# Optimization experiments

Hardware: AMD Instinct MI355X
Metric: run time of the kernel (lower is better)

## Reference

```python
import jax, jax.numpy as jnp
import numpy as np

N_NODES = 20000
N_EDGES = 320000
N_RELS = 500
EMB = 256
D4 = EMB // 4
B = 32
GAMMA = 12.0
BN_EPS = 1e-5


def _linear(x, W, b):
    return x @ W.T + b


def _bn(x, g, b, m, v):
    # BatchNorm1d in eval mode with running stats
    return (x - m) * jax.lax.rsqrt(v + BN_EPS) * g + b


def _comp_layer(src, dst, h, e, WO, bO, WI, bI, WS, bS, bng, bnb, bnm, bnv):
    # CompGCNLayer: u_sub_e message + per-node mean over in-edges ('ho')
    # and, on the reversed graph, over out-edges ('hi'); nodes with no
    # incident edges get 0 (dgl mean semantics).
    n = h.shape[0]
    ones = jnp.ones(src.shape[0], h.dtype)
    deg_in = jnp.maximum(jax.ops.segment_sum(ones, dst, num_segments=n), 1.0)
    deg_out = jnp.maximum(jax.ops.segment_sum(ones, src, num_segments=n), 1.0)
    ho = jax.ops.segment_sum(h[src] - e, dst, num_segments=n) / deg_in[:, None]
    hi = jax.ops.segment_sum(h[dst] - e, src, num_segments=n) / deg_out[:, None]
    out = (_linear(ho, WO, bO) + _linear(hi, WI, bI) + _linear(h, WS, bS)) / 3.0
    return _bn(out, bng, bnb, bnm, bnv)


def _forward(node_embs, edge_embs, params, src, dst, e_vid, hids, rids, tids,
             is_update_g_embs, is_head_pred):
    (W_O1, b_O1, W_I1, b_I1, W_S1, b_S1, bn1_g, bn1_b, bn1_m, bn1_v, Wr1, br1,
     W_O2, b_O2, W_I2, b_I2, W_S2, b_S2, bn2_g, bn2_b, bn2_m, bn2_v, Wr2, br2) = params
    if is_update_g_embs:
        he = edge_embs[e_vid]                                   # [E, D]
        h1 = jnp.tanh(_comp_layer(src, dst, node_embs, he,
                                  W_O1, b_O1, W_I1, b_I1, W_S1, b_S1,
                                  bn1_g, bn1_b, bn1_m, bn1_v))  # [N, D/4]
        he1 = jnp.tanh(_linear(he, Wr1, br1))                   # [E, D/4]
        hn = jnp.tanh(_comp_layer(src, dst, h1, he1,
                                  W_O2, b_O2, W_I2, b_I2, W_S2, b_S2,
                                  bn2_g, bn2_b, bn2_m, bn2_v))  # [N, D]
    else:
        hn = node_embs
    heads = hn[hids]
    tails = hn[tids]
    rels = _linear(jax.nn.relu(_linear(edge_embs[rids], Wr1, br1)), Wr2, br2)
    b = hids.shape[0]
    n = hn.shape[0]
    # Faithful to torch repeat_interleave indexing in predict():
    # flat element k pairs query row k//C with candidate row k//B.
    cand_idx = (jnp.arange(b)[:, None] * n + jnp.arange(n)[None, :]) // b  # [B, N]
    cand = hn[cand_idx]                                                    # [B, N, D]
    if is_head_pred == 1:
        diff = cand + (rels - tails)[:, None, :]
    else:
        diff = (heads + rels)[:, None, :] - cand
    dist = jnp.sqrt(jnp.sum(diff * diff, axis=-1))  # p = norm = 2
    score = jax.nn.sigmoid(GAMMA - dist)
    return hn, score


def setup_inputs() -> dict:
    key = jax.random.key(0)
    ks = jax.random.split(key, 20)
    w = lambda k, shp: jax.random.normal(k, shp, jnp.float32) * 0.05
    inp = {
        "node_embs": jax.random.normal(ks[0], (N_NODES, EMB), jnp.float32),
        "edge_embs": jax.random.normal(ks[1], (N_RELS, EMB), jnp.float32),
        "W_O1": w(ks[2], (D4, EMB)), "b_O1": jnp.zeros((D4,), jnp.float32),
        "W_I1": w(ks[3], (D4, EMB)), "b_I1": jnp.zeros((D4,), jnp.float32),
        "W_S1": w(ks[4], (D4, EMB)), "b_S1": jnp.zeros((D4,), jnp.float32),
        "bn1_g": jnp.ones((D4,), jnp.float32), "bn1_b": jnp.zeros((D4,), jnp.float32),
        "bn1_m": jnp.zeros((D4,), jnp.float32), "bn1_v": jnp.ones((D4,), jnp.float32),
        "Wr1": w(ks[5], (D4, EMB)), "br1": jnp.zeros((D4,), jnp.float32),
        "W_O2": w(ks[6], (EMB, D4)), "b_O2": jnp.zeros((EMB,), jnp.float32),
        "W_I2": w(ks[7], (EMB, D4)), "b_I2": jnp.zeros((EMB,), jnp.float32),
        "W_S2": w(ks[8], (EMB, D4)), "b_S2": jnp.zeros((EMB,), jnp.float32),
        "bn2_g": jnp.ones((EMB,), jnp.float32), "bn2_b": jnp.zeros((EMB,), jnp.float32),
        "bn2_m": jnp.zeros((EMB,), jnp.float32), "bn2_v": jnp.ones((EMB,), jnp.float32),
        "Wr2": w(ks[9], (EMB, D4)), "br2": jnp.zeros((EMB,), jnp.float32),
        "src": jax.random.randint(ks[10], (N_EDGES,), 0, N_NODES, jnp.int32),
        "dst": jax.random.randint(ks[11], (N_EDGES,), 0, N_NODES, jnp.int32),
        "e_vid": jax.random.randint(ks[12], (N_EDGES,), 0, N_RELS, jnp.int32),
        "hids": jax.random.randint(ks[13], (B,), 0, N_NODES, jnp.int32),
        "rids": jax.random.randint(ks[14], (B,), 0, N_RELS, jnp.int32),
        "tids": jax.random.randint(ks[15], (B,), 0, N_NODES, jnp.int32),
        "is_update_g_embs": 1,
        "is_head_pred": 0,
    }
    return inp


def reference(node_embs, edge_embs,
              W_O1, b_O1, W_I1, b_I1, W_S1, b_S1, bn1_g, bn1_b, bn1_m, bn1_v,
              Wr1, br1,
              W_O2, b_O2, W_I2, b_I2, W_S2, b_S2, bn2_g, bn2_b, bn2_m, bn2_v,
              Wr2, br2,
              src, dst, e_vid, hids, rids, tids,
              is_update_g_embs, is_head_pred):
    params = (W_O1, b_O1, W_I1, b_I1, W_S1, b_S1, bn1_g, bn1_b, bn1_m, bn1_v,
              Wr1, br1,
              W_O2, b_O2, W_I2, b_I2, W_S2, b_S2, bn2_g, bn2_b, bn2_m, bn2_v,
              Wr2, br2)
    return _forward(node_embs, edge_embs, params, src, dst, e_vid,
                    hids, rids, tids, is_update_g_embs, is_head_pred)
```

## Files before the change

kernel.cpp:

```cpp
#include <hip/hip_runtime.h>
#include <math.h>

#define NN 20000
#define NE 320000
#define NR 500
#define EMBD 256
#define D4 64
#define BQ 32
#define TOT (2 * NN)
#define NB 40

#define NBLK_HIST 1250
#define NBLK_BN 448
#define NBLK_K1 (NBLK_HIST + NBLK_BN + 2 + BQ)

#define NBLK_GC1 939
#define NBLK_GE1 32
#define NBLK_MEGA (NBLK_GC1 + NBLK_GE1 + NBLK_HIST)

typedef __attribute__((ext_vector_type(8))) short bf16x8;
typedef __attribute__((ext_vector_type(4))) float f32x4;

__device__ __forceinline__ unsigned short f2bf(float x)
{
    unsigned int u = __float_as_uint(x);
    unsigned int r = (u + 0x7fffu + ((u >> 16) & 1u)) >> 16;
    return (unsigned short)r;
}

__device__ __forceinline__ float4 bf4tof4(uint2 u)
{
    float4 r;
    r.x = __uint_as_float((u.x & 0xFFFFu) << 16);
    r.y = __uint_as_float(u.x & 0xFFFF0000u);
    r.z = __uint_as_float((u.y & 0xFFFFu) << 16);
    r.w = __uint_as_float(u.y & 0xFFFF0000u);
    return r;
}

__global__ __launch_bounds__(256) void k_prep(
    const int* __restrict__ src, const int* __restrict__ dst,
    const int* __restrict__ evid, int* __restrict__ cnt, unsigned* __restrict__ rank2,
    const float* __restrict__ W_O1, const float* __restrict__ W_I1,
    const float* __restrict__ W_S1, const float* __restrict__ Wr1,
    const float* __restrict__ W_O2, const float* __restrict__ W_I2,
    const float* __restrict__ W_S2,
    unsigned short* __restrict__ Bn1, unsigned short* __restrict__ Bn2,
    const float* __restrict__ bO1, const float* __restrict__ bI1,
    const float* __restrict__ bS1,
    const float* __restrict__ g1, const float* __restrict__ bb1,
    const float* __restrict__ m1, const float* __restrict__ v1,
    const float* __restrict__ bO2, const float* __restrict__ bI2,
    const float* __restrict__ bS2,
    const float* __restrict__ g2, const float* __restrict__ bb2,
    const float* __restrict__ m2, const float* __restrict__ v2,
    float* __restrict__ s1, float* __restrict__ t1,
    float* __restrict__ s2, float* __restrict__ t2,
    const float* __restrict__ edge_embs,
    const float* __restrict__ br1, const float* __restrict__ br2,
    const float* __restrict__ Wr2full, const int* __restrict__ rids,
    float* __restrict__ rels)
{
    int b = blockIdx.x;
    if (b < NBLK_HIST) {
        int i = b * 256 + threadIdx.x;
        if (i < NE) {
            int r_in = atomicAdd(&cnt[dst[i]], 1);
            int r_out = atomicAdd(&cnt[NN + src[i]], 1);
            rank2[i] = (unsigned)r_in | ((unsigned)r_out << 16);
        }
        return;
    }
    b -= NBLK_HIST;
    if (b < NBLK_BN) {
        int id = b * 256 + threadIdx.x;
        if (id < 256 * 256) {
            int n = id >> 8, k = id & 255;
            float v;
            if (n < 64)       v = W_O1[n * 256 + k];
            else if (n < 128) v = W_I1[(n - 64) * 256 + k];
            else if (n < 192) v = W_S1[(n - 128) * 256 + k];
            else              v = Wr1[(n - 192) * 256 + k];
            Bn1[id] = f2bf(v);
        } else {
            int id2 = id - 256 * 256;
            if (id2 < 256 * 192) {
                int n = id2 / 192, k = id2 - n * 192;
                float v;
                if (k < 64)       v = W_O2[n * 64 + k];
                else if (k < 128) v = W_I2[n * 64 + (k - 64)];
                else              v = W_S2[n * 64 + (k - 128)];
                Bn2[id2] = f2bf(v);
            }
        }
        return;
    }
    b -= NBLK_BN;
    if (b < 2) {
        int i = b * 256 + threadIdx.x;
        if (i < 64) {
            float rsg = g1[i] / sqrtf(v1[i] + 1e-5f);
            s1[i] = rsg * (1.f / 3.f);
            t1[i] = ((bO1[i] + bI1[i] + bS1[i]) * (1.f / 3.f) - m1[i]) * rsg + bb1[i];
        } else if (i < 320) {
            int n = i - 64;
            float rsg = g2[n] / sqrtf(v2[n] + 1e-5f);
            s2[n] = rsg * (1.f / 3.f);
            t2[n] = ((bO2[n] + bI2[n] + bS2[n]) * (1.f / 3.f) - m2[n]) * rsg + bb2[n];
        }
        return;
    }
    {
        __shared__ float e_s[256];
        __shared__ float m_s[64];
        int rb = b - 2, o = threadIdx.x;
        int rid = rids[rb];
        e_s[o] = edge_embs[(size_t)rid * 256 + o];
        __syncthreads();
        if (o < 64) {
            float acc = br1[o];
            for (int k = 0; k < 256; ++k) acc = fmaf(e_s[k], Wr1[o * 256 + k], acc);
            m_s[o] = fmaxf(acc, 0.f);
        }
        __syncthreads();
        float r = br2[o];
        for (int jj = 0; jj < 64; ++jj) r = fmaf(m_s[jj], Wr2full[o * 64 + jj], r);
        rels[rb * 256 + o] = r;
    }
}


__global__ __launch_bounds__(256) void k_scanA(const int* __restrict__ cnt,
                                               int* __restrict__ bsum)
{
    __shared__ int lds[256];
    int t = threadIdx.x;
    int base = blockIdx.x * 1024 + t * 4;
    int s = 0;
    if (base + 3 < TOT) {
        int4 v = *(const int4*)(cnt + base);
        s = v.x + v.y + v.z + v.w;
    } else {
        for (int c = 0; c < 4; ++c) { int i = base + c; if (i < TOT) s += cnt[i]; }
    }
    lds[t] = s;
    __syncthreads();
    for (int d = 128; d > 0; d >>= 1) {
        if (t < d) lds[t] += lds[t + d];
        __syncthreads();
    }
    if (t == 0) bsum[blockIdx.x] = lds[0];
}

__global__ __launch_bounds__(64) void k_scanB(int* __restrict__ bsum)
{
    int t = threadIdx.x;
    int v = (t < NB) ? bsum[t] : 0;
#pragma unroll
    for (int d = 1; d < 64; d <<= 1) {
        int u = __shfl_up(v, d, 64);
        if (t >= d) v += u;
    }
    int ex = __shfl_up(v, 1, 64);
    if (t == 0) ex = 0;
    if (t < NB) bsum[t] = ex;
}

__global__ __launch_bounds__(256) void k_scanC(const int* __restrict__ cnt,
                                               const int* __restrict__ bsum,
                                               int* __restrict__ offc)
{
    __shared__ int lds[256];
    int t = threadIdx.x;
    int base = blockIdx.x * 1024 + t * 4;
    int e0 = 0, e1 = 0, e2 = 0, e3 = 0;
    if (base + 3 < TOT) {
        int4 v = *(const int4*)(cnt + base);
        e0 = v.x; e1 = v.y; e2 = v.z; e3 = v.w;
    } else {
        if (base + 0 < TOT) e0 = cnt[base + 0];
        if (base + 1 < TOT) e1 = cnt[base + 1];
        if (base + 2 < TOT) e2 = cnt[base + 2];
        if (base + 3 < TOT) e3 = cnt[base + 3];
    }
    int s = e0 + e1 + e2 + e3;
    lds[t] = s;
    __syncthreads();
    for (int d = 1; d < 256; d <<= 1) {
        int u = (t >= d) ? lds[t - d] : 0;
        __syncthreads();
        lds[t] += u;
        __syncthreads();
    }
    int run = lds[t] - s + bsum[blockIdx.x];
    if (base + 3 < TOT) {
        int4 o = make_int4(run, run + e0, run + e0 + e1, run + e0 + e1 + e2);
        *(int4*)(offc + base) = o;
    } else {
        int r = run;
        if (base + 0 < TOT) { offc[base + 0] = r; r += e0; }
        if (base + 1 < TOT) { offc[base + 1] = r; r += e1; }
        if (base + 2 < TOT) { offc[base + 2] = r; r += e2; }
        if (base + 3 < TOT) { offc[base + 3] = r; r += e3; }
    }
    if (blockIdx.x == 0 && t == 0) offc[TOT] = 2 * NE;
}

__device__ __forceinline__ void gemm_dev(
    unsigned short* As, unsigned short* Bs,
    const void* __restrict__ Av, int aBf16, int M, int K, int lda,
    const unsigned short* __restrict__ Bn,
    void* __restrict__ C, int ldc, int mode,
    const float* __restrict__ sv, const float* __restrict__ tv,
    const float* __restrict__ node_embs, const int* __restrict__ flag,
    int m0, int n0)
{
    const int t = threadIdx.x;
    const int lane = t & 63, wave = t >> 6;
    const int wr = wave >> 1, wc = wave & 1;
    const int lrow = lane & 15, lkg = lane >> 4;

    f32x4 acc[2][2] = {};

    for (int kb = 0; kb < K; kb += 64) {
        if (aBf16) {
            const unsigned short* A = (const unsigned short*)Av;
#pragma unroll
            for (int it = 0; it < 2; ++it) {
                int idx = t + it * 256;
                int ko = idx & 7;
                int row = idx >> 3;
                int gm = m0 + row;
                uint4 a = make_uint4(0u, 0u, 0u, 0u);
                if (gm < M) a = *(const uint4*)(A + (size_t)gm * lda + kb + 8 * ko);
                *(uint4*)&As[row * 72 + 8 * ko] = a;
            }
        } else {
            const float* A = (const float*)Av;
#pragma unroll
            for (int it = 0; it < 4; ++it) {
                int idx = t + it * 256;
                int kq = idx & 15;
                int row = idx >> 4;
                int gm = m0 + row;
                float4 a = make_float4(0.f, 0.f, 0.f, 0.f);
                if (gm < M) a = *(const float4*)(A + (size_t)gm * lda + kb + 4 * kq);
                unsigned int p0 = (unsigned int)f2bf(a.x) | ((unsigned int)f2bf(a.y) << 16);
                unsigned int p1 = (unsigned int)f2bf(a.z) | ((unsigned int)f2bf(a.w) << 16);
                *(uint2*)&As[row * 72 + 4 * kq] = make_uint2(p0, p1);
            }
        }
#pragma unroll
        for (int it = 0; it < 2; ++it) {
            int idx = t + it * 256;
            int ko = idx & 7;
            int row = idx >> 3;
            uint4 b = *(const uint4*)(Bn + (size_t)(n0 + row) * K + kb + 8 * ko);
            *(uint4*)&Bs[row * 72 + 8 * ko] = b;
        }
        __syncthreads();
#pragma unroll
        for (int ks = 0; ks < 2; ++ks) {
            int k0 = ks * 32 + lkg * 8;
            bf16x8 af0 = *(const bf16x8*)&As[(wr * 32 + lrow) * 72 + k0];
            bf16x8 af1 = *(const bf16x8*)&As[(wr * 32 + 16 + lrow) * 72 + k0];
            bf16x8 bf0 = *(const bf16x8*)&Bs[(wc * 32 + lrow) * 72 + k0];
            bf16x8 bf1 = *(const bf16x8*)&Bs[(wc * 32 + 16 + lrow) * 72 + k0];
            acc[0][0] = __builtin_amdgcn_mfma_f32_16x16x32_bf16(af0, bf0, acc[0][0], 0, 0, 0);
            acc[0][1] = __builtin_amdgcn_mfma_f32_16x16x32_bf16(af0, bf1, acc[0][1], 0, 0, 0);
            acc[1][0] = __builtin_amdgcn_mfma_f32_16x16x32_bf16(af1, bf0, acc[1][0], 0, 0, 0);
            acc[1][1] = __builtin_amdgcn_mfma_f32_16x16x32_bf16(af1, bf1, acc[1][1], 0, 0, 0);
        }
        __syncthreads();
    }

#pragma unroll
    for (int m = 0; m < 2; ++m) {
#pragma unroll
        for (int r = 0; r < 4; ++r) {
            int gm = m0 + wr * 32 + m * 16 + lkg * 4 + r;
            if (gm >= M) continue;
#pragma unroll
            for (int n = 0; n < 2; ++n) {
                int gn = n0 + wc * 32 + n * 16 + lrow;
                float v = acc[m][n][r];
                if (mode == 0) {
                    ((unsigned short*)C)[(size_t)gm * ldc + gn] = f2bf(v);
                } else if (mode == 1) {
                    float val = (gn >= 192) ? tanhf(v + sv[gn - 192]) : v;
                    ((unsigned short*)C)[(size_t)gm * ldc + gn] = f2bf(val);
                } else {
                    float val = tanhf(v * sv[gn] + tv[gn]);
                    if (flag[0] == 0) val = node_embs[(size_t)gm * EMBD + gn];
                    ((float*)C)[(size_t)gm * EMBD + gn] = val;
                }
            }
        }
    }
}

__global__ __launch_bounds__(256) void gemm_mfma(
    const void* __restrict__ A, int aBf16, int M, int K, int lda,
    const unsigned short* __restrict__ Bn,
    void* __restrict__ C, int ldc, int mode,
    const float* __restrict__ sv, const float* __restrict__ tv,
    const float* __restrict__ node_embs, const int* __restrict__ flag)
{
    __shared__ unsigned short As[64 * 72];
    __shared__ unsigned short Bs[64 * 72];
    gemm_dev(As, Bs, A, aBf16, M, K, lda, Bn, C, ldc, mode, sv, tv, node_embs, flag,
             blockIdx.x * 64, blockIdx.y * 64);
}

__global__ __launch_bounds__(256) void k_mega(
    const float* __restrict__ node_embs, const float* __restrict__ edge_embs,
    const unsigned short* __restrict__ Bn1,
    unsigned short* __restrict__ C1b, unsigned short* __restrict__ E1b,
    const float* __restrict__ br1,
    const int* __restrict__ src, const int* __restrict__ dst,
    const int* __restrict__ evid, const unsigned* __restrict__ rank2,
    const int* __restrict__ offc, unsigned* __restrict__ R)
{
    __shared__ unsigned short As[64 * 72];
    __shared__ unsigned short Bs[64 * 72];
    int bid = blockIdx.x;
    if (bid < NBLK_GC1) {
        gemm_dev(As, Bs, node_embs, 0, NN, 256, 256, Bn1, C1b, 192, 0,
                 nullptr, nullptr, nullptr, nullptr,
                 (bid % 313) * 64, (bid / 313) * 64);
    } else if (bid < NBLK_GC1 + NBLK_GE1) {
        int b2 = bid - NBLK_GC1;
        gemm_dev(As, Bs, edge_embs, 0, NR, 256, 256, Bn1, E1b, 256, 1,
                 br1, nullptr, nullptr, nullptr,
                 (b2 % 8) * 64, (b2 / 8) * 64);
    } else {
        int e = (bid - NBLK_GC1 - NBLK_GE1) * 256 + threadIdx.x;
        if (e < NE) {
            int s = src[e], d = dst[e];
            unsigned rv = (unsigned)evid[e] << 15;
            unsigned rk = rank2[e];
            R[offc[d] + (rk & 0xFFFFu)] = (unsigned)s | rv;
            R[offc[NN + s] + (rk >> 16)] = (unsigned)d | rv;
        }
    }
}


__device__ __forceinline__ void gather_quad(
    const unsigned* __restrict__ R, int r0, int r1, int g, int q,
    const unsigned short* __restrict__ TAB, int ldt, int toff,
    const unsigned short* __restrict__ ETAB, int eoff,
    float4& acc)
{
    int lane = g * 16 + q;
    int cnt = r1 - r0;
    for (int base = 0; base < cnt; base += 64) {
        int rem = cnt - base; if (rem > 64) rem = 64;
        unsigned rec = 0u;
        if (lane < rem) rec = R[r0 + base + lane];
        int i = 0;
        for (; 4 * i + 15 < rem; i += 4) {
            unsigned ra = __shfl(rec, 4 * i + g, 64);
            unsigned rb = __shfl(rec, 4 * i + 4 + g, 64);
            unsigned rc = __shfl(rec, 4 * i + 8 + g, 64);
            unsigned rd = __shfl(rec, 4 * i + 12 + g, 64);
            uint2 ua0 = *(const uint2*)(TAB + (size_t)(ra & 0x7FFFu) * ldt + toff + 4 * q);
            uint2 ue0 = *(const uint2*)(ETAB + (size_t)(ra >> 15) * 256 + eoff + 4 * q);
            uint2 ua1 = *(const uint2*)(TAB + (size_t)(rb & 0x7FFFu) * ldt + toff + 4 * q);
            uint2 ue1 = *(const uint2*)(ETAB + (size_t)(rb >> 15) * 256 + eoff + 4 * q);
            uint2 ua2 = *(const uint2*)(TAB + (size_t)(rc & 0x7FFFu) * ldt + toff + 4 * q);
            uint2 ue2 = *(const uint2*)(ETAB + (size_t)(rc >> 15) * 256 + eoff + 4 * q);
            uint2 ua3 = *(const uint2*)(TAB + (size_t)(rd & 0x7FFFu) * ldt + toff + 4 * q);
            uint2 ue3 = *(const uint2*)(ETAB + (size_t)(rd >> 15) * 256 + eoff + 4 * q);
            float4 a0 = bf4tof4(ua0), e0 = bf4tof4(ue0);
            float4 a1 = bf4tof4(ua1), e1 = bf4tof4(ue1);
            float4 a2 = bf4tof4(ua2), e2 = bf4tof4(ue2);
            float4 a3 = bf4tof4(ua3), e3 = bf4tof4(ue3);
            acc.x += (a0.x - e0.x) + (a1.x - e1.x) + (a2.x - e2.x) + (a3.x - e3.x);
            acc.y += (a0.y - e0.y) + (a1.y - e1.y) + (a2.y - e2.y) + (a3.y - e3.y);
            acc.z += (a0.z - e0.z) + (a1.z - e1.z) + (a2.z - e2.z) + (a3.z - e3.z);
            acc.w += (a0.w - e0.w) + (a1.w - e1.w) + (a2.w - e2.w) + (a3.w - e3.w);
        }
        for (; 4 * i < rem; ++i) {
            int idx = 4 * i + g;
            unsigned rr = __shfl(rec, idx < rem ? idx : 0, 64);
            if (idx < rem) {
                uint2 ua = *(const uint2*)(TAB + (size_t)(rr & 0x7FFFu) * ldt + toff + 4 * q);
                uint2 ue = *(const uint2*)(ETAB + (size_t)(rr >> 15) * 256 + eoff + 4 * q);
                float4 a = bf4tof4(ua), e = bf4tof4(ue);
                acc.x += a.x - e.x; acc.y += a.y - e.y;
                acc.z += a.z - e.z; acc.w += a.w - e.w;
            }
        }
    }
}

__device__ __forceinline__ void xreduce(float4& v)
{
    v.x += __shfl_xor(v.x, 16, 64); v.y += __shfl_xor(v.y, 16, 64);
    v.z += __shfl_xor(v.z, 16, 64); v.w += __shfl_xor(v.w, 16, 64);
    v.x += __shfl_xor(v.x, 32, 64); v.y += __shfl_xor(v.y, 32, 64);
    v.z += __shfl_xor(v.z, 32, 64); v.w += __shfl_xor(v.w, 32, 64);
}

__device__ __forceinline__ uint2 packbf4(float4 o)
{
    return make_uint2((unsigned)f2bf(o.x) | ((unsigned)f2bf(o.y) << 16),
                      (unsigned)f2bf(o.z) | ((unsigned)f2bf(o.w) << 16));
}

__global__ __launch_bounds__(256) void k_gather1(
    const int* __restrict__ offc, const unsigned* __restrict__ R,
    const unsigned short* __restrict__ C1b, const unsigned short* __restrict__ E1b,
    const float* __restrict__ s1, const float* __restrict__ t1,
    unsigned short* __restrict__ A2b)
{
    int n = blockIdx.x * 4 + (threadIdx.x >> 6);
    if (n >= NN) return;
    int lane = threadIdx.x & 63, g = lane >> 4, q = lane & 15;
    int b0 = offc[n], b1 = offc[n + 1];
    int c0 = offc[NN + n], c1 = offc[NN + n + 1];
    float di = 1.f / fmaxf((float)(b1 - b0), 1.f);
    float dh = 1.f / fmaxf((float)(c1 - c0), 1.f);
    float4 accO = make_float4(0.f, 0.f, 0.f, 0.f);
    float4 accI = make_float4(0.f, 0.f, 0.f, 0.f);
    gather_quad(R, b0, b1, g, q, C1b, 192, 0, E1b, 0, accO);
    gather_quad(R, c0, c1, g, q, C1b, 192, 64, E1b, 64, accI);
    xreduce(accO);
    xreduce(accI);
    if (g == 0) {
        float4 hs = bf4tof4(*(const uint2*)(C1b + (size_t)n * 192 + 128 + 4 * q));
        float4 sv = *(const float4*)(s1 + 4 * q);
        float4 tv = *(const float4*)(t1 + 4 * q);
        float4 o;
        o.x = tanhf((accO.x * di + accI.x * dh + hs.x) * sv.x + tv.x);
        o.y = tanhf((accO.y * di + accI.y * dh + hs.y) * sv.y + tv.y);
        o.z = tanhf((accO.z * di + accI.z * dh + hs.z) * sv.z + tv.z);
        o.w = tanhf((accO.w * di + accI.w * dh + hs.w) * sv.w + tv.w);
        *(uint2*)(A2b + (size_t)n * 192 + 128 + 4 * q) = packbf4(o);
    }
}

__global__ __launch_bounds__(256) void k_gather2(
    const int* __restrict__ offc, const unsigned* __restrict__ R,
    const unsigned short* __restrict__ A2r, const unsigned short* __restrict__ E1b,
    unsigned short* __restrict__ A2w)
{
    int n = blockIdx.x * 4 + (threadIdx.x >> 6);
    if (n >= NN) return;
    int lane = threadIdx.x & 63, g = lane >> 4, q = lane & 15;
    int b0 = offc[n], b1 = offc[n + 1];
    int c0 = offc[NN + n], c1 = offc[NN + n + 1];
    float di = 1.f / fmaxf((float)(b1 - b0), 1.f);
    float dh = 1.f / fmaxf((float)(c1 - c0), 1.f);
    float4 accO = make_float4(0.f, 0.f, 0.f, 0.f);
    float4 accI = make_float4(0.f, 0.f, 0.f, 0.f);
    gather_quad(R, b0, b1, g, q, A2r, 192, 128, E1b, 192, accO);
    gather_quad(R, c0, c1, g, q, A2r, 192, 128, E1b, 192, accI);
    xreduce(accO);
    xreduce(accI);
    if (g == 0) {
        float4 o0, o1;
        o0.x = accO.x * di; o0.y = accO.y * di; o0.z = accO.z * di; o0.w = accO.w * di;
        o1.x = accI.x * dh; o1.y = accI.y * dh; o1.z = accI.z * dh; o1.w = accI.w * dh;
        *(uint2*)(A2w + (size_t)n * 192 + 4 * q) = packbf4(o0);
        *(uint2*)(A2w + (size_t)n * 192 + 64 + 4 * q) = packbf4(o1);
    }
}

__global__ __launch_bounds__(256) void k_tvec(
    const float* __restrict__ rels, const float* __restrict__ hn,
    const int* __restrict__ hids, const int* __restrict__ tids,
    const int* __restrict__ is_head, float* __restrict__ tvec)
{
    int b = blockIdx.x, o = threadIdx.x;
    int ih = is_head[0];
    int nid = ih ? tids[b] : hids[b];
    float r = rels[b * 256 + o];
    float hv = hn[(size_t)nid * 256 + o];
    tvec[b * 256 + o] = ih ? (hv - r) : (hv + r);
}

__global__ __launch_bounds__(256) void k_score(
    const float* __restrict__ hn, const float* __restrict__ tvec,
    float* __restrict__ score)
{
    int p = blockIdx.x * 4 + (threadIdx.x >> 6);
    if (p >= BQ * (NN / BQ)) return;
    int l = threadIdx.x & 63;
    int b = p / (NN / BQ);
    int j = p - b * (NN / BQ);
    int idx = (b * NN + 32 * j) / BQ;
    float ssum = 0.f;
#pragma unroll
    for (int q = 0; q < 4; ++q) {
        float df = hn[(size_t)idx * 256 + l + 64 * q] - tvec[b * 256 + l + 64 * q];
        ssum = fmaf(df, df, ssum);
    }
#pragma unroll
    for (int off = 32; off >= 1; off >>= 1) ssum += __shfl_xor(ssum, off, 64);
    float dist = sqrtf(ssum);
    float sc = 1.f / (1.f + expf(dist - 12.f));
    if (l < 32) score[(size_t)b * NN + 32 * j + l] = sc;
}

extern "C" void kernel_launch(void* const* d_in, const int* in_sizes, int n_in,
                              void* d_out, int out_size, void* d_ws, size_t ws_size,
                              hipStream_t stream)
{
    const float* node_embs = (const float*)d_in[0];
    const float* edge_embs = (const float*)d_in[1];
    const float* W_O1 = (const float*)d_in[2];  const float* b_O1 = (const float*)d_in[3];
    const float* W_I1 = (const float*)d_in[4];  const float* b_I1 = (const float*)d_in[5];
    const float* W_S1 = (const float*)d_in[6];  const float* b_S1 = (const float*)d_in[7];
    const float* bn1_g = (const float*)d_in[8]; const float* bn1_b = (const float*)d_in[9];
    const float* bn1_m = (const float*)d_in[10];const float* bn1_v = (const float*)d_in[11];
    const float* Wr1 = (const float*)d_in[12];  const float* br1 = (const float*)d_in[13];
    const float* W_O2 = (const float*)d_in[14]; const float* b_O2 = (const float*)d_in[15];
    const float* W_I2 = (const float*)d_in[16]; const float* b_I2 = (const float*)d_in[17];
    const float* W_S2 = (const float*)d_in[18]; const float* b_S2 = (const float*)d_in[19];
    const float* bn2_g = (const float*)d_in[20];const float* bn2_b = (const float*)d_in[21];
    const float* bn2_m = (const float*)d_in[22];const float* bn2_v = (const float*)d_in[23];
    const float* Wr2 = (const float*)d_in[24];  const float* br2 = (const float*)d_in[25];
    const int* src = (const int*)d_in[26];
    const int* dst = (const int*)d_in[27];
    const int* evid = (const int*)d_in[28];
    const int* hids = (const int*)d_in[29];
    const int* rids = (const int*)d_in[30];
    const int* tids = (const int*)d_in[31];
    const int* upd = (const int*)d_in[32];
    const int* ihead = (const int*)d_in[33];

    unsigned short* C1b = (unsigned short*)d_ws;
    unsigned short* A2b = C1b + 3840000;
    unsigned short* E1b = A2b + 3840000;
    unsigned short* Bn1 = E1b + 128000;
    unsigned short* Bn2 = Bn1 + 65536;

    float* s1   = (float*)(Bn2 + 49152);
    float* t1   = s1 + 64;
    float* s2   = t1 + 64;
    float* t2   = s2 + 256;
    float* rels = t2 + 256;
    float* tvec = rels + 8192;

    unsigned* R     = (unsigned*)(tvec + 8192);
    unsigned* rank2 = R + 2 * NE;
    int* cnt    = (int*)(rank2 + NE);
    int* offc   = cnt + TOT;
    int* bsum   = offc + TOT + 1;

    float* hn    = (float*)d_out;
    float* score = hn + (size_t)NN * EMBD;

    hipMemsetAsync(cnt, 0, (size_t)TOT * 4, stream);

    k_prep<<<NBLK_K1, 256, 0, stream>>>(
        src, dst, evid, cnt, rank2,
        W_O1, W_I1, W_S1, Wr1, W_O2, W_I2, W_S2, Bn1, Bn2,
        b_O1, b_I1, b_S1, bn1_g, bn1_b, bn1_m, bn1_v,
        b_O2, b_I2, b_S2, bn2_g, bn2_b, bn2_m, bn2_v,
        s1, t1, s2, t2,
        edge_embs, br1, br2, Wr2, rids, rels);

    k_scanA<<<NB, 256, 0, stream>>>(cnt, bsum);
    k_scanB<<<1, 64, 0, stream>>>(bsum);
    k_scanC<<<NB, 256, 0, stream>>>(cnt, bsum, offc);

    k_mega<<<NBLK_MEGA, 256, 0, stream>>>(node_embs, edge_embs, Bn1,
                                          C1b, E1b, br1, src, dst, evid, rank2, offc, R);

    k_gather1<<<NN / 4, 256, 0, stream>>>(offc, R, C1b, E1b, s1, t1, A2b);
    k_gather2<<<NN / 4, 256, 0, stream>>>(offc, R, A2b, E1b, A2b);

    gemm_mfma<<<dim3(313, 4), 256, 0, stream>>>(A2b, 1, NN, 192, 192, Bn2,
                                                hn, 256, 2, s2, t2, node_embs, upd);

    k_tvec<<<BQ, 256, 0, stream>>>(rels, hn, hids, tids, ihead, tvec);
    k_score<<<(BQ * (NN / BQ)) / 4, 256, 0, stream>>>(hn, tvec, score);
}
```

Measured before the change: 143.2 us.

## Merge scan kernels via grid barrier, fuse tvec into score, reorder mega blocks

Replaces the three-kernel prefix scan with one kernel in which blocks publish their sums and spin on an atomic counter before each computes its own exclusive prefix. The tvec kernel is folded into the scoring kernel, which now rebuilds the query vector inline. Inside the mega kernel, the edge-scatter blocks are moved ahead of the GEMM blocks so they get scheduled first. Together these remove three launches and a small intermediate buffer, at the cost of redundant rels/hn loads in scoring. The spin barrier depends on all 40 scan blocks being resident at the same time.

```diff
diff --git a/kernel.cpp b/kernel.cpp
--- a/kernel.cpp
+++ b/kernel.cpp
@@ -16,7 +16,7 @@
 
 #define NBLK_GC1 939
 #define NBLK_GE1 32
-#define NBLK_MEGA (NBLK_GC1 + NBLK_GE1 + NBLK_HIST)
+#define NBLK_MEGA (NBLK_HIST + NBLK_GE1 + NBLK_GC1)
 
 typedef __attribute__((ext_vector_type(8))) short bf16x8;
 typedef __attribute__((ext_vector_type(4))) float f32x4;
@@ -40,7 +40,7 @@
 
 __global__ __launch_bounds__(256) void k_prep(
     const int* __restrict__ src, const int* __restrict__ dst,
-    const int* __restrict__ evid, int* __restrict__ cnt, unsigned* __restrict__ rank2,
+    int* __restrict__ cnt, unsigned* __restrict__ rank2,
     const float* __restrict__ W_O1, const float* __restrict__ W_I1,
     const float* __restrict__ W_S1, const float* __restrict__ Wr1,
     const float* __restrict__ W_O2, const float* __restrict__ W_I2,
@@ -129,50 +129,15 @@
     }
 }
 
-
-__global__ __launch_bounds__(256) void k_scanA(const int* __restrict__ cnt,
-                                               int* __restrict__ bsum)
+__global__ __launch_bounds__(256) void k_scan(const int* __restrict__ cnt,
+                                              int* __restrict__ off_bin,
+                                              int* __restrict__ bsum,
+                                              int* __restrict__ flag)
 {
     __shared__ int lds[256];
-    int t = threadIdx.x;
-    int base = blockIdx.x * 1024 + t * 4;
-    int s = 0;
-    if (base + 3 < TOT) {
-        int4 v = *(const int4*)(cnt + base);
-        s = v.x + v.y + v.z + v.w;
-    } else {
-        for (int c = 0; c < 4; ++c) { int i = base + c; if (i < TOT) s += cnt[i]; }
-    }
-    lds[t] = s;
-    __syncthreads();
-    for (int d = 128; d > 0; d >>= 1) {
-        if (t < d) lds[t] += lds[t + d];
-        __syncthreads();
-    }
-    if (t == 0) bsum[blockIdx.x] = lds[0];
-}
-
-__global__ __launch_bounds__(64) void k_scanB(int* __restrict__ bsum)
-{
-    int t = threadIdx.x;
-    int v = (t < NB) ? bsum[t] : 0;
-#pragma unroll
-    for (int d = 1; d < 64; d <<= 1) {
-        int u = __shfl_up(v, d, 64);
-        if (t >= d) v += u;
-    }
-    int ex = __shfl_up(v, 1, 64);
-    if (t == 0) ex = 0;
-    if (t < NB) bsum[t] = ex;
-}
-
-__global__ __launch_bounds__(256) void k_scanC(const int* __restrict__ cnt,
-                                               const int* __restrict__ bsum,
-                                               int* __restrict__ offc)
-{
-    __shared__ int lds[256];
-    int t = threadIdx.x;
-    int base = blockIdx.x * 1024 + t * 4;
+    __shared__ int pre_s;
+    int t = threadIdx.x, bid = blockIdx.x;
+    int base = bid * 1024 + t * 4;
     int e0 = 0, e1 = 0, e2 = 0, e3 = 0;
     if (base + 3 < TOT) {
         int4 v = *(const int4*)(cnt + base);
@@ -192,18 +157,35 @@
         lds[t] += u;
         __syncthreads();
     }
-    int run = lds[t] - s + bsum[blockIdx.x];
+    if (t == 255) {
+        bsum[bid] = lds[255];
+        __threadfence();
+        atomicAdd(flag, 1);
+    }
+    if (t == 0) {
+        while (atomicAdd(flag, 0) < NB) { }
+    }
+    __syncthreads();
+    __threadfence();
+    if (t < 64) {
+        int v = (t < bid) ? atomicAdd(&bsum[t], 0) : 0;
+#pragma unroll
+        for (int d = 32; d >= 1; d >>= 1) v += __shfl_xor(v, d, 64);
+        if (t == 0) pre_s = v;
+    }
+    __syncthreads();
+    int run = lds[t] - s + pre_s;
     if (base + 3 < TOT) {
         int4 o = make_int4(run, run + e0, run + e0 + e1, run + e0 + e1 + e2);
-        *(int4*)(offc + base) = o;
+        *(int4*)(off_bin + base) = o;
     } else {
         int r = run;
-        if (base + 0 < TOT) { offc[base + 0] = r; r += e0; }
-        if (base + 1 < TOT) { offc[base + 1] = r; r += e1; }
-        if (base + 2 < TOT) { offc[base + 2] = r; r += e2; }
-        if (base + 3 < TOT) { offc[base + 3] = r; r += e3; }
-    }
-    if (blockIdx.x == 0 && t == 0) offc[TOT] = 2 * NE;
+        if (base + 0 < TOT) { off_bin[base + 0] = r; r += e0; }
+        if (base + 1 < TOT) { off_bin[base + 1] = r; r += e1; }
+        if (base + 2 < TOT) { off_bin[base + 2] = r; r += e2; }
+        if (base + 3 < TOT) { off_bin[base + 3] = r; r += e3; }
+    }
+    if (bid == 0 && t == 0) off_bin[TOT] = 2 * NE;
 }
 
 __device__ __forceinline__ void gemm_dev(
@@ -324,17 +306,8 @@
     __shared__ unsigned short As[64 * 72];
     __shared__ unsigned short Bs[64 * 72];
     int bid = blockIdx.x;
-    if (bid < NBLK_GC1) {
-        gemm_dev(As, Bs, node_embs, 0, NN, 256, 256, Bn1, C1b, 192, 0,
-                 nullptr, nullptr, nullptr, nullptr,
-                 (bid % 313) * 64, (bid / 313) * 64);
-    } else if (bid < NBLK_GC1 + NBLK_GE1) {
-        int b2 = bid - NBLK_GC1;
-        gemm_dev(As, Bs, edge_embs, 0, NR, 256, 256, Bn1, E1b, 256, 1,
-                 br1, nullptr, nullptr, nullptr,
-                 (b2 % 8) * 64, (b2 / 8) * 64);
-    } else {
-        int e = (bid - NBLK_GC1 - NBLK_GE1) * 256 + threadIdx.x;
+    if (bid < NBLK_HIST) {
+        int e = bid * 256 + threadIdx.x;
         if (e < NE) {
             int s = src[e], d = dst[e];
             unsigned rv = (unsigned)evid[e] << 15;
@@ -342,6 +315,18 @@
             R[offc[d] + (rk & 0xFFFFu)] = (unsigned)s | rv;
             R[offc[NN + s] + (rk >> 16)] = (unsigned)d | rv;
         }
+        return;
+    }
+    int b2 = bid - NBLK_HIST;
+    if (b2 < NBLK_GE1) {
+        gemm_dev(As, Bs, edge_embs, 0, NR, 256, 256, Bn1, E1b, 256, 1,
+                 br1, nullptr, nullptr, nullptr,
+                 (b2 % 8) * 64, (b2 / 8) * 64);
+    } else {
+        int b3 = b2 - NBLK_GE1;
+        gemm_dev(As, Bs, node_embs, 0, NN, 256, 256, Bn1, C1b, 192, 0,
+                 nullptr, nullptr, nullptr, nullptr,
+                 (b3 % 313) * 64, (b3 / 313) * 64);
     }
 }
 
@@ -468,22 +453,10 @@
     }
 }
 
-__global__ __launch_bounds__(256) void k_tvec(
-    const float* __restrict__ rels, const float* __restrict__ hn,
+__global__ __launch_bounds__(256) void k_score(
+    const float* __restrict__ hn, const float* __restrict__ rels,
     const int* __restrict__ hids, const int* __restrict__ tids,
-    const int* __restrict__ is_head, float* __restrict__ tvec)
-{
-    int b = blockIdx.x, o = threadIdx.x;
-    int ih = is_head[0];
-    int nid = ih ? tids[b] : hids[b];
-    float r = rels[b * 256 + o];
-    float hv = hn[(size_t)nid * 256 + o];
-    tvec[b * 256 + o] = ih ? (hv - r) : (hv + r);
-}
-
-__global__ __launch_bounds__(256) void k_score(
-    const float* __restrict__ hn, const float* __restrict__ tvec,
-    float* __restrict__ score)
+    const int* __restrict__ is_head, float* __restrict__ score)
 {
     int p = blockIdx.x * 4 + (threadIdx.x >> 6);
     if (p >= BQ * (NN / BQ)) return;
@@ -491,10 +464,15 @@
     int b = p / (NN / BQ);
     int j = p - b * (NN / BQ);
     int idx = (b * NN + 32 * j) / BQ;
+    int ih = is_head[0];
+    int nid = ih ? tids[b] : hids[b];
     float ssum = 0.f;
 #pragma unroll
     for (int q = 0; q < 4; ++q) {
-        float df = hn[(size_t)idx * 256 + l + 64 * q] - tvec[b * 256 + l + 64 * q];
+        float r = rels[b * 256 + l + 64 * q];
+        float hv = hn[(size_t)nid * 256 + l + 64 * q];
+        float tv = ih ? (hv - r) : (hv + r);
+        float df = hn[(size_t)idx * 256 + l + 64 * q] - tv;
         ssum = fmaf(df, df, ssum);
     }
 #pragma unroll
@@ -542,40 +520,37 @@
     float* s2   = t1 + 64;
     float* t2   = s2 + 256;
     float* rels = t2 + 256;
-    float* tvec = rels + 8192;
-
-    unsigned* R     = (unsigned*)(tvec + 8192);
+
+    unsigned* R     = (unsigned*)(rels + 8192);
     unsigned* rank2 = R + 2 * NE;
     int* cnt    = (int*)(rank2 + NE);
-    int* offc   = cnt + TOT;
-    int* bsum   = offc + TOT + 1;
+    int* flag   = cnt + TOT;
+    int* off_bin= flag + 1;
+    int* bsum   = off_bin + TOT + 1;
 
     float* hn    = (float*)d_out;
     float* score = hn + (size_t)NN * EMBD;
 
-    hipMemsetAsync(cnt, 0, (size_t)TOT * 4, stream);
+    hipMemsetAsync(cnt, 0, (size_t)(TOT + 1) * 4, stream);
 
     k_prep<<<NBLK_K1, 256, 0, stream>>>(
-        src, dst, evid, cnt, rank2,
+        src, dst, cnt, rank2,
         W_O1, W_I1, W_S1, Wr1, W_O2, W_I2, W_S2, Bn1, Bn2,
         b_O1, b_I1, b_S1, bn1_g, bn1_b, bn1_m, bn1_v,
         b_O2, b_I2, b_S2, bn2_g, bn2_b, bn2_m, bn2_v,
         s1, t1, s2, t2,
         edge_embs, br1, br2, Wr2, rids, rels);
 
-    k_scanA<<<NB, 256, 0, stream>>>(cnt, bsum);
-    k_scanB<<<1, 64, 0, stream>>>(bsum);
-    k_scanC<<<NB, 256, 0, stream>>>(cnt, bsum, offc);
+    k_scan<<<NB, 256, 0, stream>>>(cnt, off_bin, bsum, flag);
 
     k_mega<<<NBLK_MEGA, 256, 0, stream>>>(node_embs, edge_embs, Bn1,
-                                          C1b, E1b, br1, src, dst, evid, rank2, offc, R);
-
-    k_gather1<<<NN / 4, 256, 0, stream>>>(offc, R, C1b, E1b, s1, t1, A2b);
-    k_gather2<<<NN / 4, 256, 0, stream>>>(offc, R, A2b, E1b, A2b);
+                                          C1b, E1b, br1, src, dst, evid, rank2, off_bin, R);
+
+    k_gather1<<<NN / 4, 256, 0, stream>>>(off_bin, R, C1b, E1b, s1, t1, A2b);
+    k_gather2<<<NN / 4, 256, 0, stream>>>(off_bin, R, A2b, E1b, A2b);
 
     gemm_mfma<<<dim3(313, 4), 256, 0, stream>>>(A2b, 1, NN, 192, 192, Bn2,
                                                 hn, 256, 2, s2, t2, node_embs, upd);
 
-    k_tvec<<<BQ, 256, 0, stream>>>(rels, hn, hids, tids, ihead, tvec);
-    k_score<<<(BQ * (NN / BQ)) / 4, 256, 0, stream>>>(hn, tvec, score);
-}
+    k_score<<<(BQ * (NN / BQ)) / 4, 256, 0, stream>>>(hn, rels, hids, tids, ihead, score);
+}
```

After: 144.5 us. Within noise of the previous version (+0.9%).
